# Optimization experiments

Hardware: AMD Instinct MI355X
Metric: run time of the kernel (lower is better)

## Reference

```python
import jax, jax.numpy as jnp
import numpy as np

N_NODES = 50000
N_EDGES = 800000
D = 128  # node_dim == edge_dim
NEG_SLOPE = 0.2


def setup_inputs() -> dict:
    key = jax.random.key(0)
    ks = jax.random.split(key, 16)
    w = lambda k, shp: (jax.random.normal(k, shp, dtype=jnp.float32) * 0.02)
    b = lambda: jnp.zeros((D,), dtype=jnp.float32)
    return {
        "V": jax.random.normal(ks[0], (N_NODES, D), dtype=jnp.float32),
        "E": jax.random.normal(ks[1], (N_EDGES, D), dtype=jnp.float32),
        "src": jax.random.randint(ks[2], (N_EDGES,), 0, N_NODES, dtype=jnp.int32),
        "dst": jax.random.randint(ks[3], (N_EDGES,), 0, N_NODES, dtype=jnp.int32),
        # NodePooling: two node_dim->node_dim linears
        "Wp1": w(ks[4], (D, D)), "bp1": b(),
        "Wp2": w(ks[5], (D, D)), "bp2": b(),
        # GenMessage.A: MLP with nb_mlp_layer=2 linears (edge_dim->edge_dim)
        "WA1": w(ks[6], (D, D)), "bA1": b(),
        "WA2": w(ks[7], (D, D)), "bA2": b(),
        # GenMessage.B (scale) and .C (shift): edge_dim->node_dim
        "WB": w(ks[8], (D, D)), "bB": b(),
        "WC": w(ks[9], (D, D)), "bC": b(),
    }


def reference(V, E, src, dst, Wp1, bp1, Wp2, bp2, WA1, bA1, WA2, bA2, WB, bB, WC, bC):
    lrelu = lambda x: jax.nn.leaky_relu(x, NEG_SLOPE)
    # V = act(V); G.ndata['V'] = pooling(V)
    Vp = lrelu(lrelu(V) @ Wp1.T + bp1) @ Wp2.T + bp2  # [N, D]
    # edge MLP on edge features (ReLU between linears, none after last)
    x = jax.nn.relu(E @ WA1.T + bA1) @ WA2.T + bA2    # [E, D]
    scale = jax.nn.sigmoid(x @ WB.T + bB)             # [E, D]
    shift = x @ WC.T + bC                             # [E, D]
    # per-edge gated message using gathered source node features
    msg = scale * Vp[src] + shift                     # [E, D]
    # scatter-sum into destination nodes (dgl.fn.sum)
    out = jax.ops.segment_sum(msg, dst, num_segments=N_NODES)  # [N, D]
    return out
```

## Files before the change

### kernel.cpp

```cpp
#include <hip/hip_runtime.h>
#include <hip/hip_bf16.h>

typedef __attribute__((ext_vector_type(8))) short bf16x8;
typedef __attribute__((ext_vector_type(4))) float f32x4;

#define DD 128

static __device__ __forceinline__ unsigned short f2bf(float f) {
    __bf16 h = (__bf16)f;
    return __builtin_bit_cast(unsigned short, h);
}
static __device__ __forceinline__ unsigned int pk2bf(float lo, float hi) {
    return ((unsigned int)f2bf(hi) << 16) | (unsigned int)f2bf(lo);
}
static __device__ __forceinline__ float bf2f(unsigned short h) {
    unsigned int u = ((unsigned int)h) << 16;
    return __builtin_bit_cast(float, u);
}

static __device__ __forceinline__ void lds_barrier() {
    asm volatile("s_waitcnt lgkmcnt(0)" ::: "memory");
    __builtin_amdgcn_s_barrier();
    asm volatile("" ::: "memory");
}

__global__ __launch_bounds__(256) void k_convert_hist(
    const float* __restrict__ w0, const float* __restrict__ w1,
    const float* __restrict__ w2, const float* __restrict__ w3,
    const float* __restrict__ w4, const float* __restrict__ w5,
    unsigned short* __restrict__ wbf,
    const int* __restrict__ dst, int* __restrict__ counts, int nE, int use_perm) {
    int i = blockIdx.x * blockDim.x + threadIdx.x;
    if (i < 6 * 16384) {
        int m = i >> 14, k = i & 16383;
        const float* s = (m == 0) ? w0 : (m == 1) ? w1 : (m == 2) ? w2 : (m == 3) ? w3
                         : (m == 4) ? w4 : w5;
        wbf[i] = f2bf(s[k]);
    }
    if (use_perm)
        for (int e = i; e < nE; e += gridDim.x * blockDim.x)
            atomicAdd(&counts[dst[e]], 1);
}

__global__ __launch_bounds__(1024) void k_scan(const int* __restrict__ counts,
                                               int* __restrict__ cursor, int nN) {
    __shared__ int ps[1024];
    const int tid = threadIdx.x;
    if ((nN & 3) == 0) {
        const int nQ = nN >> 2;
        const int chunk = (nQ + 1023) / 1024;
        const int q0 = tid * chunk;
        const int4* c4 = (const int4*)counts;
        int s = 0;
#pragma unroll 4
        for (int i = 0; i < chunk; ++i) {
            int q = q0 + i;
            if (q < nQ) { int4 v = c4[q]; s += v.x + v.y + v.z + v.w; }
        }
        ps[tid] = s;
        __syncthreads();
        for (int off = 1; off < 1024; off <<= 1) {
            int add = (tid >= off) ? ps[tid - off] : 0;
            __syncthreads();
            ps[tid] += add;
            __syncthreads();
        }
        int run = (tid > 0) ? ps[tid - 1] : 0;
        int4* cur4 = (int4*)cursor;
#pragma unroll 4
        for (int i = 0; i < chunk; ++i) {
            int q = q0 + i;
            if (q < nQ) {
                int4 v = c4[q], w;
                w.x = run; run += v.x;
                w.y = run; run += v.y;
                w.z = run; run += v.z;
                w.w = run; run += v.w;
                cur4[q] = w;
            }
        }
    } else {
        const int chunk = (nN + 1023) / 1024;
        const int base = tid * chunk;
        int s = 0;
        for (int i = 0; i < chunk; ++i) {
            int idx = base + i;
            s += (idx < nN) ? counts[idx] : 0;
        }
        ps[tid] = s;
        __syncthreads();
        for (int off = 1; off < 1024; off <<= 1) {
            int add = (tid >= off) ? ps[tid - off] : 0;
            __syncthreads();
            ps[tid] += add;
            __syncthreads();
        }
        int run = (tid > 0) ? ps[tid - 1] : 0;
        for (int i = 0; i < chunk; ++i) {
            int idx = base + i;
            if (idx < nN) { cursor[idx] = run; run += counts[idx]; }
        }
    }
}

__global__ __launch_bounds__(256, 3) void k_nodes(
    const float* __restrict__ V, const unsigned short* __restrict__ wbf,
    const float* __restrict__ bp1, const float* __restrict__ bp2,
    unsigned short* __restrict__ Vp, int nN, int nTiles,
    const int* __restrict__ dst, int* __restrict__ cursor,
    int* __restrict__ perm, int nE, int use_perm)
{
    if (use_perm)
        for (int e = blockIdx.x * blockDim.x + threadIdx.x; e < nE; e += gridDim.x * blockDim.x) {
            int pos = atomicAdd(&cursor[dst[e]], 1);
            perm[pos] = e;
        }

    const int lane = threadIdx.x & 63;
    const int wave = threadIdx.x >> 6;
    const int lr = lane & 15, lg = lane >> 4;

    bf16x8 B1[2][4], B2[2][4];
#pragma unroll
    for (int ct = 0; ct < 2; ++ct)
#pragma unroll
        for (int kk = 0; kk < 4; ++kk) {
            int j = wave * 32 + ct * 16 + lr;
            int k0 = kk * 32 + lg * 8;
            B1[ct][kk] = *(const bf16x8*)(wbf + 0 * 16384 + j * DD + k0);
            B2[ct][kk] = *(const bf16x8*)(wbf + 1 * 16384 + j * DD + k0);
        }
    float b1v[2], b2v[2];
#pragma unroll
    for (int ct = 0; ct < 2; ++ct) {
        int c = wave * 32 + ct * 16 + lr;
        b1v[ct] = bp1[c]; b2v[ct] = bp2[c];
    }
    __shared__ alignas(16) unsigned short xb[32][136];

    for (int t = blockIdx.x; t < nTiles; t += gridDim.x) {
        const int r0 = t * 32;
        bf16x8 A[2][4];
#pragma unroll
        for (int rg = 0; rg < 2; ++rg)
#pragma unroll
            for (int kk = 0; kk < 4; ++kk) {
                int row = r0 + rg * 16 + lr; if (row >= nN) row = nN - 1;
                const float4* p = (const float4*)(V + (size_t)row * DD + kk * 32 + lg * 8);
                float4 f0 = p[0], f1 = p[1];
                float v[8] = {f0.x, f0.y, f0.z, f0.w, f1.x, f1.y, f1.z, f1.w};
                bf16x8 a;
#pragma unroll
                for (int e = 0; e < 8; ++e) {
                    float x = v[e];
                    x = x > 0.f ? x : 0.2f * x;
                    a[e] = (short)f2bf(x);
                }
                A[rg][kk] = a;
            }
#pragma unroll
        for (int rg = 0; rg < 2; ++rg)
#pragma unroll
            for (int ct = 0; ct < 2; ++ct) {
                f32x4 acc = {0.f, 0.f, 0.f, 0.f};
#pragma unroll
                for (int kk = 0; kk < 4; ++kk)
                    acc = __builtin_amdgcn_mfma_f32_16x16x32_bf16(A[rg][kk], B1[ct][kk], acc, 0, 0, 0);
#pragma unroll
                for (int r = 0; r < 4; ++r) {
                    float x = acc[r] + b1v[ct];
                    x = x > 0.f ? x : 0.2f * x;
                    xb[rg * 16 + lg * 4 + r][wave * 32 + ct * 16 + lr] = f2bf(x);
                }
            }
        lds_barrier();
        bf16x8 A2[2][4];
#pragma unroll
        for (int rg = 0; rg < 2; ++rg)
#pragma unroll
            for (int kk = 0; kk < 4; ++kk)
                A2[rg][kk] = *(const bf16x8*)&xb[rg * 16 + lr][kk * 32 + lg * 8];
#pragma unroll
        for (int rg = 0; rg < 2; ++rg)
#pragma unroll
            for (int ct = 0; ct < 2; ++ct) {
                f32x4 acc = {0.f, 0.f, 0.f, 0.f};
#pragma unroll
                for (int kk = 0; kk < 4; ++kk)
                    acc = __builtin_amdgcn_mfma_f32_16x16x32_bf16(A2[rg][kk], B2[ct][kk], acc, 0, 0, 0);
#pragma unroll
                for (int r = 0; r < 4; ++r) {
                    int row = r0 + rg * 16 + lg * 4 + r;
                    if (row < nN)
                        Vp[(size_t)row * DD + wave * 32 + ct * 16 + lr] = f2bf(acc[r] + b2v[ct]);
                }
            }
        lds_barrier();
    }
}

__global__ __launch_bounds__(256, 2) void k_edges(
    const float* __restrict__ E, const int* __restrict__ src, const int* __restrict__ dst,
    const int* __restrict__ perm, int use_perm,
    const unsigned short* __restrict__ wbf,
    const float* __restrict__ bA1, const float* __restrict__ bA2,
    const float* __restrict__ bB, const float* __restrict__ bC,
    const unsigned short* __restrict__ Vp, float* __restrict__ out, int nE, int nTiles)
{
    const int lane = threadIdx.x & 63;
    const int wave = threadIdx.x >> 6;
    const int lr = lane & 15, lg = lane >> 4;
    const int srow = threadIdx.x >> 3;
    const int schunk = threadIdx.x & 7;

    bf16x8 B1[2][4], B2[2][4], B3[2][4], B4[2][4];
#pragma unroll
    for (int ct = 0; ct < 2; ++ct)
#pragma unroll
        for (int kk = 0; kk < 4; ++kk) {
            int j = wave * 32 + ct * 16 + lr;
            int k0 = kk * 32 + lg * 8;
            const unsigned short* p = wbf + 2 * 16384 + j * DD + k0;
            B1[ct][kk] = *(const bf16x8*)(p);
            B2[ct][kk] = *(const bf16x8*)(p + 16384);
            B3[ct][kk] = *(const bf16x8*)(p + 32768);
            B4[ct][kk] = *(const bf16x8*)(p + 49152);
        }
    float b1v[2], b2v[2], b3v[2], b4v[2];
#pragma unroll
    for (int ct = 0; ct < 2; ++ct) {
        int c = wave * 32 + ct * 16 + lr;
        b1v[ct] = bA1[c]; b2v[ct] = bA2[c]; b3v[ct] = bB[c]; b4v[ct] = bC[c];
    }
    __shared__ alignas(16) unsigned short xb[2][32][136];
    __shared__ alignas(16) unsigned short Eb[2][32][136];
    __shared__ alignas(8)  unsigned short gv[32][132];
    __shared__ alignas(16) float msgb[32][132];
    __shared__ int dstb[33];

    const int gstep = gridDim.x;
    int t = blockIdx.x;

    auto pidx = [&](int i) -> int {
        if (i >= nE) i = nE - 1;
        return use_perm ? perm[i] : i;
    };

    int pe_t = pidx(t * 32 + srow);
    int pe1  = pidx((t + gstep) * 32 + srow);
    uint2 g0, g1, g2, g3;
    {
        const uint2* vp2 = (const uint2*)(Vp + (size_t)src[pe_t] * DD);
        g0 = vp2[schunk]; g1 = vp2[schunk + 8]; g2 = vp2[schunk + 16]; g3 = vp2[schunk + 24];
    }
    int pd = ((t * 32 + srow) < nE) ? dst[pe_t] : -1;
    float4 pf0, pf1, pf2, pf3;
    {
        const float4* np = (const float4*)(E + (size_t)pe1 * DD + schunk * 16);
        pf0 = np[0]; pf1 = np[1]; pf2 = np[2]; pf3 = np[3];
    }
    {
        const float4* p = (const float4*)(E + (size_t)pe_t * DD + schunk * 16);
        float4 f0 = p[0], f1 = p[1], f2 = p[2], f3 = p[3];
        uint4 w0 = make_uint4(pk2bf(f0.x, f0.y), pk2bf(f0.z, f0.w),
                              pk2bf(f1.x, f1.y), pk2bf(f1.z, f1.w));
        uint4 w1 = make_uint4(pk2bf(f2.x, f2.y), pk2bf(f2.z, f2.w),
                              pk2bf(f3.x, f3.y), pk2bf(f3.z, f3.w));
        uint4* wp = (uint4*)&Eb[0][srow][schunk * 16];
        wp[0] = w0; wp[1] = w1;
    }
    lds_barrier();
    int cur = 0;

    for (; t < nTiles; t += gstep) {
        bf16x8 A[2][4];
#pragma unroll
        for (int rg = 0; rg < 2; ++rg)
#pragma unroll
            for (int kk = 0; kk < 4; ++kk)
                A[rg][kk] = *(const bf16x8*)&Eb[cur][rg * 16 + lr][kk * 32 + lg * 8];
#pragma unroll
        for (int rg = 0; rg < 2; ++rg)
#pragma unroll
            for (int ct = 0; ct < 2; ++ct) {
                f32x4 acc = {0.f, 0.f, 0.f, 0.f};
#pragma unroll
                for (int kk = 0; kk < 4; ++kk)
                    acc = __builtin_amdgcn_mfma_f32_16x16x32_bf16(A[rg][kk], B1[ct][kk], acc, 0, 0, 0);
#pragma unroll
                for (int r = 0; r < 4; ++r) {
                    float x = fmaxf(acc[r] + b1v[ct], 0.f);
                    xb[0][rg * 16 + lg * 4 + r][wave * 32 + ct * 16 + lr] = f2bf(x);
                }
            }
        lds_barrier();
        *(uint2*)&gv[srow][schunk * 4]      = g0;
        *(uint2*)&gv[srow][schunk * 4 + 32] = g1;
        *(uint2*)&gv[srow][schunk * 4 + 64] = g2;
        *(uint2*)&gv[srow][schunk * 4 + 96] = g3;
        if (schunk == 0) dstb[srow] = pd;
        int pe2 = pidx((t + 2 * gstep) * 32 + srow);
        float4 nf0, nf1, nf2, nf3;
        {
            const float4* np = (const float4*)(E + (size_t)pe2 * DD + schunk * 16);
            nf0 = np[0]; nf1 = np[1]; nf2 = np[2]; nf3 = np[3];
        }
        {
            int sl = src[pe1];
            const uint2* nvp2 = (const uint2*)(Vp + (size_t)sl * DD);
            g0 = nvp2[schunk]; g1 = nvp2[schunk + 8]; g2 = nvp2[schunk + 16]; g3 = nvp2[schunk + 24];
        }
        int pdn = (((t + gstep) * 32 + srow) < nE) ? dst[pe1] : -1;
        bf16x8 A2[2][4];
#pragma unroll
        for (int rg = 0; rg < 2; ++rg)
#pragma unroll
            for (int kk = 0; kk < 4; ++kk)
                A2[rg][kk] = *(const bf16x8*)&xb[0][rg * 16 + lr][kk * 32 + lg * 8];
#pragma unroll
        for (int rg = 0; rg < 2; ++rg)
#pragma unroll
            for (int ct = 0; ct < 2; ++ct) {
                f32x4 acc = {0.f, 0.f, 0.f, 0.f};
#pragma unroll
                for (int kk = 0; kk < 4; ++kk)
                    acc = __builtin_amdgcn_mfma_f32_16x16x32_bf16(A2[rg][kk], B2[ct][kk], acc, 0, 0, 0);
#pragma unroll
                for (int r = 0; r < 4; ++r)
                    xb[1][rg * 16 + lg * 4 + r][wave * 32 + ct * 16 + lr] = f2bf(acc[r] + b2v[ct]);
            }
        lds_barrier();
        {
            uint4 w0 = make_uint4(pk2bf(pf0.x, pf0.y), pk2bf(pf0.z, pf0.w),
                                  pk2bf(pf1.x, pf1.y), pk2bf(pf1.z, pf1.w));
            uint4 w1 = make_uint4(pk2bf(pf2.x, pf2.y), pk2bf(pf2.z, pf2.w),
                                  pk2bf(pf3.x, pf3.y), pk2bf(pf3.z, pf3.w));
            uint4* wp = (uint4*)&Eb[cur ^ 1][srow][schunk * 16];
            wp[0] = w0; wp[1] = w1;
        }
        bf16x8 A3[2][4];
#pragma unroll
        for (int rg = 0; rg < 2; ++rg)
#pragma unroll
            for (int kk = 0; kk < 4; ++kk)
                A3[rg][kk] = *(const bf16x8*)&xb[1][rg * 16 + lr][kk * 32 + lg * 8];
#pragma unroll
        for (int rg = 0; rg < 2; ++rg)
#pragma unroll
            for (int ct = 0; ct < 2; ++ct) {
                f32x4 aB = {0.f, 0.f, 0.f, 0.f}, aC = {0.f, 0.f, 0.f, 0.f};
#pragma unroll
                for (int kk = 0; kk < 4; ++kk) {
                    aB = __builtin_amdgcn_mfma_f32_16x16x32_bf16(A3[rg][kk], B3[ct][kk], aB, 0, 0, 0);
                    aC = __builtin_amdgcn_mfma_f32_16x16x32_bf16(A3[rg][kk], B4[ct][kk], aC, 0, 0, 0);
                }
                const int col = wave * 32 + ct * 16 + lr;
#pragma unroll
                for (int r = 0; r < 4; ++r) {
                    float e = __expf(-(aB[r] + b3v[ct]));
                    float sc = __builtin_amdgcn_rcpf(1.f + e);
                    float sh = aC[r] + b4v[ct];
                    float v = bf2f(gv[rg * 16 + lg * 4 + r][col]);
                    msgb[rg * 16 + lg * 4 + r][col] = sc * v + sh;
                }
            }
        lds_barrier();
        {
            const int col = threadIdx.x & 127;
            const int half = threadIdx.x >> 7;
            float acc = 0.f;
#pragma unroll
            for (int r = half * 16; r < half * 16 + 16; ++r) {
                acc += msgb[r][col];
                bool flush = (r == half * 16 + 15) || (dstb[r + 1] != dstb[r]);
                if (flush) {
                    int d = dstb[r];
                    if (d >= 0)
                        unsafeAtomicAdd(out + (size_t)d * DD + col, acc);
                    acc = 0.f;
                }
            }
        }
        cur ^= 1;
        pf0 = nf0; pf1 = nf1; pf2 = nf2; pf3 = nf3;
        pe1 = pe2; pd = pdn;
    }
}

extern "C" void kernel_launch(void* const* d_in, const int* in_sizes, int n_in,
                              void* d_out, int out_size, void* d_ws, size_t ws_size,
                              hipStream_t stream) {
    const float* V   = (const float*)d_in[0];
    const float* E   = (const float*)d_in[1];
    const int*   src = (const int*)d_in[2];
    const int*   dst = (const int*)d_in[3];
    const float* Wp1 = (const float*)d_in[4];  const float* bp1 = (const float*)d_in[5];
    const float* Wp2 = (const float*)d_in[6];  const float* bp2 = (const float*)d_in[7];
    const float* WA1 = (const float*)d_in[8];  const float* bA1 = (const float*)d_in[9];
    const float* WA2 = (const float*)d_in[10]; const float* bA2 = (const float*)d_in[11];
    const float* WB  = (const float*)d_in[12]; const float* bB  = (const float*)d_in[13];
    const float* WC  = (const float*)d_in[14]; const float* bC  = (const float*)d_in[15];
    float* out = (float*)d_out;

    const int nN = in_sizes[0] / DD;
    const int nE = in_sizes[1] / DD;
    const int nTilesN = (nN + 31) / 32;
    const int nTilesE = (nE + 31) / 32;

    char* wsb = (char*)d_ws;
    unsigned short* wbf = (unsigned short*)wsb;
    unsigned short* Vp  = (unsigned short*)(wsb + 196608);
    size_t off_counts = 196608 + (size_t)nN * 256;
    int* counts = (int*)(wsb + off_counts);
    int* cursor = (int*)(wsb + off_counts + (size_t)nN * 4);
    int* perm   = (int*)(wsb + off_counts + (size_t)nN * 8);
    size_t ws_need = off_counts + (size_t)nN * 8 + (size_t)nE * 4;
    int use_perm = (ws_size >= ws_need) ? 1 : 0;

    hipMemsetAsync(d_out, 0, (size_t)out_size * sizeof(float), stream);
    if (use_perm) hipMemsetAsync(counts, 0, (size_t)nN * 4, stream);

    k_convert_hist<<<1024, 256, 0, stream>>>(Wp1, Wp2, WA1, WA2, WB, WC, wbf,
                                             dst, counts, nE, use_perm);
    if (use_perm) k_scan<<<1, 1024, 0, stream>>>(counts, cursor, nN);

    int gN = nTilesN < 768 ? nTilesN : 768;
    k_nodes<<<gN, 256, 0, stream>>>(V, wbf, bp1, bp2, Vp, nN, nTilesN,
                                    dst, cursor, perm, nE, use_perm);
    int gE = nTilesE < 512 ? nTilesE : 512;
    k_edges<<<gE, 256, 0, stream>>>(E, src, dst, perm, use_perm, wbf,
                                    bA1, bA2, bB, bC, Vp, out, nE, nTilesE);
}
```

Measured before the change: 360.7 us.

## Parallelize prefix scan and segment-reduce messages in registers via shuffles

Replaces the single-block 1024-thread scan over node counts with a two-kernel multi-block scan (per-block scan plus partial-offset add). In the edge kernel, messages stay in registers and are segment-summed across lane groups with shuffle carries instead of being staged through a shared-memory buffer and an extra barrier. The E-tile bf16 store is also moved ahead of the next-tile prefetch and second GEMM. Trade-offs are an extra kernel launch, redundant partial summation in scanB, and more atomics per flush, since each lane now issues two column atomics.

After: 353.0 us. 2.1% less time.

```diff
diff --git a/kernel.cpp b/kernel.cpp
--- a/kernel.cpp
+++ b/kernel.cpp
@@ -42,65 +42,43 @@
             atomicAdd(&counts[dst[e]], 1);
 }
 
-__global__ __launch_bounds__(1024) void k_scan(const int* __restrict__ counts,
-                                               int* __restrict__ cursor, int nN) {
-    __shared__ int ps[1024];
+__global__ __launch_bounds__(256) void k_scanA(const int* __restrict__ counts,
+                                               int* __restrict__ cursor,
+                                               int* __restrict__ partials, int nN) {
+    __shared__ int ps[256];
     const int tid = threadIdx.x;
-    if ((nN & 3) == 0) {
-        const int nQ = nN >> 2;
-        const int chunk = (nQ + 1023) / 1024;
-        const int q0 = tid * chunk;
-        const int4* c4 = (const int4*)counts;
-        int s = 0;
-#pragma unroll 4
-        for (int i = 0; i < chunk; ++i) {
-            int q = q0 + i;
-            if (q < nQ) { int4 v = c4[q]; s += v.x + v.y + v.z + v.w; }
-        }
-        ps[tid] = s;
+    const int i = blockIdx.x * 256 + tid;
+    int v = (i < nN) ? counts[i] : 0;
+    ps[tid] = v;
+    __syncthreads();
+    for (int off = 1; off < 256; off <<= 1) {
+        int add = (tid >= off) ? ps[tid - off] : 0;
         __syncthreads();
-        for (int off = 1; off < 1024; off <<= 1) {
-            int add = (tid >= off) ? ps[tid - off] : 0;
-            __syncthreads();
-            ps[tid] += add;
-            __syncthreads();
-        }
-        int run = (tid > 0) ? ps[tid - 1] : 0;
-        int4* cur4 = (int4*)cursor;
-#pragma unroll 4
-        for (int i = 0; i < chunk; ++i) {
-            int q = q0 + i;
-            if (q < nQ) {
-                int4 v = c4[q], w;
-                w.x = run; run += v.x;
-                w.y = run; run += v.y;
-                w.z = run; run += v.z;
-                w.w = run; run += v.w;
-                cur4[q] = w;
-            }
-        }
-    } else {
-        const int chunk = (nN + 1023) / 1024;
-        const int base = tid * chunk;
-        int s = 0;
-        for (int i = 0; i < chunk; ++i) {
-            int idx = base + i;
-            s += (idx < nN) ? counts[idx] : 0;
-        }
-        ps[tid] = s;
+        ps[tid] += add;
         __syncthreads();
-        for (int off = 1; off < 1024; off <<= 1) {
-            int add = (tid >= off) ? ps[tid - off] : 0;
-            __syncthreads();
-            ps[tid] += add;
-            __syncthreads();
-        }
-        int run = (tid > 0) ? ps[tid - 1] : 0;
-        for (int i = 0; i < chunk; ++i) {
-            int idx = base + i;
-            if (idx < nN) { cursor[idx] = run; run += counts[idx]; }
-        }
-    }
+    }
+    if (i < nN) cursor[i] = ps[tid] - v;
+    if (tid == 255) partials[blockIdx.x] = ps[255];
+}
+
+__global__ __launch_bounds__(256) void k_scanB(int* __restrict__ cursor,
+                                               const int* __restrict__ partials,
+                                               int nN, int nB) {
+    __shared__ int ps[256];
+    const int tid = threadIdx.x;
+    int v = 0;
+    for (int j = tid; j < blockIdx.x; j += 256) v += partials[j];
+    ps[tid] = v;
+    __syncthreads();
+    for (int off = 1; off < 256; off <<= 1) {
+        int add = (tid >= off) ? ps[tid - off] : 0;
+        __syncthreads();
+        ps[tid] += add;
+        __syncthreads();
+    }
+    const int offset = ps[255];
+    const int i = blockIdx.x * 256 + tid;
+    if (i < nN) cursor[i] += offset;
 }
 
 __global__ __launch_bounds__(256, 3) void k_nodes(
@@ -235,8 +213,7 @@
     __shared__ alignas(16) unsigned short xb[2][32][136];
     __shared__ alignas(16) unsigned short Eb[2][32][136];
     __shared__ alignas(8)  unsigned short gv[32][132];
-    __shared__ alignas(16) float msgb[32][132];
-    __shared__ int dstb[33];
+    __shared__ int dstb[32];
 
     const int gstep = gridDim.x;
     int t = blockIdx.x;
@@ -299,37 +276,6 @@
         *(uint2*)&gv[srow][schunk * 4 + 64] = g2;
         *(uint2*)&gv[srow][schunk * 4 + 96] = g3;
         if (schunk == 0) dstb[srow] = pd;
-        int pe2 = pidx((t + 2 * gstep) * 32 + srow);
-        float4 nf0, nf1, nf2, nf3;
-        {
-            const float4* np = (const float4*)(E + (size_t)pe2 * DD + schunk * 16);
-            nf0 = np[0]; nf1 = np[1]; nf2 = np[2]; nf3 = np[3];
-        }
-        {
-            int sl = src[pe1];
-            const uint2* nvp2 = (const uint2*)(Vp + (size_t)sl * DD);
-            g0 = nvp2[schunk]; g1 = nvp2[schunk + 8]; g2 = nvp2[schunk + 16]; g3 = nvp2[schunk + 24];
-        }
-        int pdn = (((t + gstep) * 32 + srow) < nE) ? dst[pe1] : -1;
-        bf16x8 A2[2][4];
-#pragma unroll
-        for (int rg = 0; rg < 2; ++rg)
-#pragma unroll
-            for (int kk = 0; kk < 4; ++kk)
-                A2[rg][kk] = *(const bf16x8*)&xb[0][rg * 16 + lr][kk * 32 + lg * 8];
-#pragma unroll
-        for (int rg = 0; rg < 2; ++rg)
-#pragma unroll
-            for (int ct = 0; ct < 2; ++ct) {
-                f32x4 acc = {0.f, 0.f, 0.f, 0.f};
-#pragma unroll
-                for (int kk = 0; kk < 4; ++kk)
-                    acc = __builtin_amdgcn_mfma_f32_16x16x32_bf16(A2[rg][kk], B2[ct][kk], acc, 0, 0, 0);
-#pragma unroll
-                for (int r = 0; r < 4; ++r)
-                    xb[1][rg * 16 + lg * 4 + r][wave * 32 + ct * 16 + lr] = f2bf(acc[r] + b2v[ct]);
-            }
-        lds_barrier();
         {
             uint4 w0 = make_uint4(pk2bf(pf0.x, pf0.y), pk2bf(pf0.z, pf0.w),
                                   pk2bf(pf1.x, pf1.y), pk2bf(pf1.z, pf1.w));
@@ -338,12 +284,44 @@
             uint4* wp = (uint4*)&Eb[cur ^ 1][srow][schunk * 16];
             wp[0] = w0; wp[1] = w1;
         }
+        int pe2 = pidx((t + 2 * gstep) * 32 + srow);
+        float4 nf0, nf1, nf2, nf3;
+        {
+            const float4* np = (const float4*)(E + (size_t)pe2 * DD + schunk * 16);
+            nf0 = np[0]; nf1 = np[1]; nf2 = np[2]; nf3 = np[3];
+        }
+        {
+            int sl = src[pe1];
+            const uint2* nvp2 = (const uint2*)(Vp + (size_t)sl * DD);
+            g0 = nvp2[schunk]; g1 = nvp2[schunk + 8]; g2 = nvp2[schunk + 16]; g3 = nvp2[schunk + 24];
+        }
+        int pdn = (((t + gstep) * 32 + srow) < nE) ? dst[pe1] : -1;
+        bf16x8 A2[2][4];
+#pragma unroll
+        for (int rg = 0; rg < 2; ++rg)
+#pragma unroll
+            for (int kk = 0; kk < 4; ++kk)
+                A2[rg][kk] = *(const bf16x8*)&xb[0][rg * 16 + lr][kk * 32 + lg * 8];
+#pragma unroll
+        for (int rg = 0; rg < 2; ++rg)
+#pragma unroll
+            for (int ct = 0; ct < 2; ++ct) {
+                f32x4 acc = {0.f, 0.f, 0.f, 0.f};
+#pragma unroll
+                for (int kk = 0; kk < 4; ++kk)
+                    acc = __builtin_amdgcn_mfma_f32_16x16x32_bf16(A2[rg][kk], B2[ct][kk], acc, 0, 0, 0);
+#pragma unroll
+                for (int r = 0; r < 4; ++r)
+                    xb[1][rg * 16 + lg * 4 + r][wave * 32 + ct * 16 + lr] = f2bf(acc[r] + b2v[ct]);
+            }
+        lds_barrier();
         bf16x8 A3[2][4];
 #pragma unroll
         for (int rg = 0; rg < 2; ++rg)
 #pragma unroll
             for (int kk = 0; kk < 4; ++kk)
                 A3[rg][kk] = *(const bf16x8*)&xb[1][rg * 16 + lr][kk * 32 + lg * 8];
+        float mA0[4], mA1[4], mB0[4], mB1[4];
 #pragma unroll
         for (int rg = 0; rg < 2; ++rg)
 #pragma unroll
@@ -361,23 +339,64 @@
                     float sc = __builtin_amdgcn_rcpf(1.f + e);
                     float sh = aC[r] + b4v[ct];
                     float v = bf2f(gv[rg * 16 + lg * 4 + r][col]);
-                    msgb[rg * 16 + lg * 4 + r][col] = sc * v + sh;
-                }
-            }
-        lds_barrier();
+                    float m = sc * v + sh;
+                    if (rg == 0) { if (ct == 0) mA0[r] = m; else mA1[r] = m; }
+                    else         { if (ct == 0) mB0[r] = m; else mB1[r] = m; }
+                }
+            }
         {
-            const int col = threadIdx.x & 127;
-            const int half = threadIdx.x >> 7;
-            float acc = 0.f;
-#pragma unroll
-            for (int r = half * 16; r < half * 16 + 16; ++r) {
-                acc += msgb[r][col];
-                bool flush = (r == half * 16 + 15) || (dstb[r + 1] != dstb[r]);
-                if (flush) {
-                    int d = dstb[r];
-                    if (d >= 0)
-                        unsafeAtomicAdd(out + (size_t)d * DD + col, acc);
-                    acc = 0.f;
+            const int col0 = wave * 32 + lr;
+            const int col1 = wave * 32 + 16 + lr;
+            int cdA = -1, cdB = -1;
+            float cvA0 = 0.f, cvA1 = 0.f, cvB0 = 0.f, cvB1 = 0.f;
+#pragma unroll
+            for (int s = 0; s < 4; ++s) {
+                int   ndA  = __shfl_up(cdA, 16, 64);
+                float nvA0 = __shfl_up(cvA0, 16, 64);
+                float nvA1 = __shfl_up(cvA1, 16, 64);
+                int   ndB  = __shfl_up(cdB, 16, 64);
+                float nvB0 = __shfl_up(cvB0, 16, 64);
+                float nvB1 = __shfl_up(cvB1, 16, 64);
+                if (lg == s) {
+                    if (s == 0) { ndA = -2; ndB = -2; }
+                    int dA[5], dB[5];
+#pragma unroll
+                    for (int r = 0; r < 4; ++r) {
+                        dA[r] = dstb[s * 4 + r];
+                        dB[r] = dstb[16 + s * 4 + r];
+                    }
+                    dA[4] = (s < 3) ? dstb[s * 4 + 4]      : -2147483647;
+                    dB[4] = (s < 3) ? dstb[16 + s * 4 + 4] : -2147483647;
+                    float a0 = (ndA == dA[0]) ? nvA0 : 0.f;
+                    float a1 = (ndA == dA[0]) ? nvA1 : 0.f;
+#pragma unroll
+                    for (int r = 0; r < 4; ++r) {
+                        a0 += mA0[r]; a1 += mA1[r];
+                        if (dA[r + 1] != dA[r]) {
+                            if (dA[r] >= 0) {
+                                unsafeAtomicAdd(out + (size_t)dA[r] * DD + col0, a0);
+                                unsafeAtomicAdd(out + (size_t)dA[r] * DD + col1, a1);
+                            }
+                            a0 = 0.f; a1 = 0.f;
+                        }
+                    }
+                    cdA = (dA[4] == dA[3]) ? dA[3] : -2;
+                    cvA0 = a0; cvA1 = a1;
+                    float b0 = (ndB == dB[0]) ? nvB0 : 0.f;
+                    float b1 = (ndB == dB[0]) ? nvB1 : 0.f;
+#pragma unroll
+                    for (int r = 0; r < 4; ++r) {
+                        b0 += mB0[r]; b1 += mB1[r];
+                        if (dB[r + 1] != dB[r]) {
+                            if (dB[r] >= 0) {
+                                unsafeAtomicAdd(out + (size_t)dB[r] * DD + col0, b0);
+                                unsafeAtomicAdd(out + (size_t)dB[r] * DD + col1, b1);
+                            }
+                            b0 = 0.f; b1 = 0.f;
+                        }
+                    }
+                    cdB = (dB[4] == dB[3]) ? dB[3] : -2;
+                    cvB0 = b0; cvB1 = b1;
                 }
             }
         }
@@ -406,15 +425,17 @@
     const int nE = in_sizes[1] / DD;
     const int nTilesN = (nN + 31) / 32;
     const int nTilesE = (nE + 31) / 32;
+    const int nB = (nN + 255) / 256;
 
     char* wsb = (char*)d_ws;
     unsigned short* wbf = (unsigned short*)wsb;
     unsigned short* Vp  = (unsigned short*)(wsb + 196608);
     size_t off_counts = 196608 + (size_t)nN * 256;
-    int* counts = (int*)(wsb + off_counts);
-    int* cursor = (int*)(wsb + off_counts + (size_t)nN * 4);
-    int* perm   = (int*)(wsb + off_counts + (size_t)nN * 8);
-    size_t ws_need = off_counts + (size_t)nN * 8 + (size_t)nE * 4;
+    int* counts   = (int*)(wsb + off_counts);
+    int* cursor   = (int*)(wsb + off_counts + (size_t)nN * 4);
+    int* perm     = (int*)(wsb + off_counts + (size_t)nN * 8);
+    int* partials = (int*)(wsb + off_counts + (size_t)nN * 8 + (size_t)nE * 4);
+    size_t ws_need = off_counts + (size_t)nN * 8 + (size_t)nE * 4 + (size_t)nB * 4;
     int use_perm = (ws_size >= ws_need) ? 1 : 0;
 
     hipMemsetAsync(d_out, 0, (size_t)out_size * sizeof(float), stream);
@@ -422,7 +443,10 @@
 
     k_convert_hist<<<1024, 256, 0, stream>>>(Wp1, Wp2, WA1, WA2, WB, WC, wbf,
                                              dst, counts, nE, use_perm);
-    if (use_perm) k_scan<<<1, 1024, 0, stream>>>(counts, cursor, nN);
+    if (use_perm) {
+        k_scanA<<<nB, 256, 0, stream>>>(counts, cursor, partials, nN);
+        k_scanB<<<nB, 256, 0, stream>>>(cursor, partials, nN, nB);
+    }
 
     int gN = nTilesN < 768 ? nTilesN : 768;
     k_nodes<<<gN, 256, 0, stream>>>(V, wbf, bp1, bp2, Vp, nN, nTilesN,
```
